# Kernel optimization log

Measured on AMD Instinct MI355X. Metric: run time of the kernel, lower is better.

## Reference

```python
import jax, jax.numpy as jnp
import numpy as np

B, L, D = 4, 1024, 1024
E, H = 8, 4096          # num_experts, mlp hidden = 4*D
CAPACITY = 6            # kthvalue rank factor: expert_k = B*L*CAPACITY


def setup_inputs() -> dict:
    key = jax.random.key(0)
    ks = jax.random.split(key, 6)
    x = jax.random.normal(ks[0], (B, L, D), dtype=jnp.float32)
    gate_weight = jax.random.normal(ks[1], (E, D), dtype=jnp.float32) * 0.006
    w1 = jax.random.normal(ks[2], (E, H, D), dtype=jnp.float32) * 0.02
    b1 = jnp.zeros((E, H), dtype=jnp.float32)
    w2 = jax.random.normal(ks[3], (E, D, H), dtype=jnp.float32) * 0.02
    b2 = jnp.zeros((E, D), dtype=jnp.float32)
    return {"x": x, "gate_weight": gate_weight, "w1": w1, "b1": b1, "w2": w2, "b2": b2}


def reference(x, gate_weight, w1, b1, w2, b2):
    # Router: logits [B, L, E]
    logits = jnp.einsum('bld,ed->ble', x, gate_weight)
    # Global kth-smallest threshold over all B*L*E token-expert logits
    expert_k = B * L * CAPACITY
    kth_val = jnp.sort(logits.reshape(-1))[expert_k - 1]
    mask = (logits >= kth_val).astype(x.dtype)
    gates = logits * mask  # identity gate * boolean mask
    # Dense per-expert MLP on every token: [B, L, E, H] hidden
    h = jax.nn.gelu(jnp.einsum('bld,ehd->bleh', x, w1) + b1, approximate=True)
    # Expert outputs stacked along last dim: [B, L, D, E]
    y = jnp.einsum('bleh,edh->blde', h, w2) + b2.T[None, None]
    # Weighted sum combine over experts
    out = jnp.einsum('blde,ble->bld', y, gates)
    return out
```

## Files before the change

kernel.cpp:

```cpp
#include <hip/hip_runtime.h>
#include <hip/hip_bf16.h>

#define TT 4096
#define DD 1024
#define EE 8
#define HH 4096
#define KSEL 24576
#define HS  1536

using f32x4 = __attribute__((ext_vector_type(4))) float;
using s16x8 = __attribute__((ext_vector_type(8))) short;

__device__ __forceinline__ unsigned short f2bf(float f) {
    unsigned int u = __float_as_uint(f);
    unsigned int r = u + 0x7FFFu + ((u >> 16) & 1u);
    return (unsigned short)(r >> 16);
}

__device__ __forceinline__ float gelu_tanh(float v) {
    float v3 = v * v * v;
    return 0.5f * v * (1.0f + tanhf(0.7978845608028654f * (v + 0.044715f * v3)));
}

__device__ __forceinline__ s16x8 cvt8(float4 a, float4 b) {
    s16x8 r;
    r[0] = (short)f2bf(a.x); r[1] = (short)f2bf(a.y);
    r[2] = (short)f2bf(a.z); r[3] = (short)f2bf(a.w);
    r[4] = (short)f2bf(b.x); r[5] = (short)f2bf(b.y);
    r[6] = (short)f2bf(b.z); r[7] = (short)f2bf(b.w);
    return r;
}

__global__ void k_logits(const float* __restrict__ x, const float* __restrict__ gw,
                         float* __restrict__ logits) {
    int wid = threadIdx.x >> 6, lane = threadIdx.x & 63;
    int t = blockIdx.x * 4 + wid;
    if (t >= TT) return;
    const float* xr = x + (size_t)t * DD;
    float acc[EE];
#pragma unroll
    for (int e = 0; e < EE; ++e) acc[e] = 0.f;
    for (int i = 0; i < DD / 64; ++i) {
        int d = i * 64 + lane;
        float xv = xr[d];
#pragma unroll
        for (int e = 0; e < EE; ++e) acc[e] += xv * gw[e * DD + d];
    }
#pragma unroll
    for (int e = 0; e < EE; ++e) {
        float v = acc[e];
        for (int off = 32; off; off >>= 1) v += __shfl_xor(v, off, 64);
        if (lane == 0) logits[(size_t)t * EE + e] = v;
    }
}

__global__ void k_select(const float* __restrict__ logits, float* __restrict__ kth) {
    int tid = threadIdx.x;
    unsigned int v[32];
#pragma unroll
    for (int i = 0; i < 32; ++i) {
        unsigned int b = __float_as_uint(logits[tid + i * 1024]);
        v[i] = (b & 0x80000000u) ? ~b : (b | 0x80000000u);
    }
    __shared__ int s_cnt;
    unsigned int prefix = 0;
    for (int bit = 31; bit >= 0; --bit) {
        unsigned int cand = prefix | (1u << bit);
        int c = 0;
#pragma unroll
        for (int i = 0; i < 32; ++i) c += (v[i] < cand) ? 1 : 0;
        for (int off = 32; off; off >>= 1) c += __shfl_xor(c, off, 64);
        __syncthreads();
        if (tid == 0) s_cnt = 0;
        __syncthreads();
        if ((tid & 63) == 0) atomicAdd(&s_cnt, c);
        __syncthreads();
        if (s_cnt < KSEL) prefix = cand;
    }
    if (tid == 0) {
        unsigned int b = (prefix & 0x80000000u) ? (prefix ^ 0x80000000u) : ~prefix;
        *kth = __uint_as_float(b);
    }
}

__global__ void k_lists(const float* __restrict__ logits, const float* __restrict__ kth,
                        int* __restrict__ cnt, int* __restrict__ toks,
                        float* __restrict__ gates) {
    int idx = blockIdx.x * 256 + threadIdx.x;
    float v = logits[idx];
    if (v >= *kth) {
        int e = idx & 7, t = idx >> 3;
        int p = atomicAdd(&cnt[e], 1);
        if (p < TT) { toks[e * TT + p] = t; gates[e * TT + p] = v; }
    }
}


#define SWZ_W(r, cb) ((r) * 64 + ((cb) ^ (((r) & 3) << 4)))

__global__ __launch_bounds__(256, 2) void k_mlp1(
    const float* __restrict__ x, const float* __restrict__ w1,
    const float* __restrict__ b1, const int* __restrict__ cnt,
    const int* __restrict__ toks, unsigned short* __restrict__ h_ws) {
    int e = blockIdx.z;
    int c = cnt[e];
    int m0 = blockIdx.x * 128;
    if (m0 >= c) return;
    int n0 = blockIdx.y * 128;

    __shared__ char sA[2][8192];
    __shared__ char sB[2][8192];

    int tid = threadIdx.x;
    int w = tid >> 6, lane = tid & 63;
    int l15 = lane & 15, l4 = lane >> 4;
    int wrow = (w >> 1) * 64, wcol = (w & 1) * 64;

    int ra = tid >> 1, ha = tid & 1;
    int ptok = m0 + ra;
    int tok = (ptok < c) ? toks[e * TT + ptok] : 0;
    const float* srcA = x + (size_t)tok * DD + ha * 16;
    const float* srcB = w1 + ((size_t)e * HH + n0 + ra) * DD + ha * 16;
    int wbyteA0 = SWZ_W(ra, ha * 32);
    int wbyteA1 = SWZ_W(ra, ha * 32 + 16);

    f32x4 acc[4][4];
#pragma unroll
    for (int mf = 0; mf < 4; ++mf)
#pragma unroll
        for (int nf = 0; nf < 4; ++nf) acc[mf][nf] = (f32x4){0.f, 0.f, 0.f, 0.f};

    int rchunk = ((l4 ^ (l15 & 3)) * 16);

    float4 la[4], lb[4];
#pragma unroll
    for (int q = 0; q < 4; ++q) { la[q] = ((const float4*)srcA)[q]; lb[q] = ((const float4*)srcB)[q]; }
    *(s16x8*)(&sA[0][wbyteA0]) = cvt8(la[0], la[1]);
    *(s16x8*)(&sA[0][wbyteA1]) = cvt8(la[2], la[3]);
    *(s16x8*)(&sB[0][wbyteA0]) = cvt8(lb[0], lb[1]);
    *(s16x8*)(&sB[0][wbyteA1]) = cvt8(lb[2], lb[3]);
    __syncthreads();

    const int NS = DD / 32;
    for (int s = 0; s < NS; ++s) {
        if (s + 1 < NS) {
            const float* pa = srcA + (s + 1) * 32;
            const float* pb = srcB + (s + 1) * 32;
#pragma unroll
            for (int q = 0; q < 4; ++q) { la[q] = ((const float4*)pa)[q]; lb[q] = ((const float4*)pb)[q]; }
        }
        int buf = s & 1;
        s16x8 af[4], bf[4];
#pragma unroll
        for (int mf = 0; mf < 4; ++mf) {
            int r = wrow + mf * 16 + l15;
            af[mf] = *(const s16x8*)(&sA[buf][r * 64 + rchunk]);
        }
#pragma unroll
        for (int nf = 0; nf < 4; ++nf) {
            int r = wcol + nf * 16 + l15;
            bf[nf] = *(const s16x8*)(&sB[buf][r * 64 + rchunk]);
        }
#pragma unroll
        for (int mf = 0; mf < 4; ++mf)
#pragma unroll
            for (int nf = 0; nf < 4; ++nf)
                acc[mf][nf] = __builtin_amdgcn_mfma_f32_16x16x32_bf16(af[mf], bf[nf], acc[mf][nf], 0, 0, 0);
        if (s + 1 < NS) {
            int nb = buf ^ 1;
            *(s16x8*)(&sA[nb][wbyteA0]) = cvt8(la[0], la[1]);
            *(s16x8*)(&sA[nb][wbyteA1]) = cvt8(la[2], la[3]);
            *(s16x8*)(&sB[nb][wbyteA0]) = cvt8(lb[0], lb[1]);
            *(s16x8*)(&sB[nb][wbyteA1]) = cvt8(lb[2], lb[3]);
        }
        __syncthreads();
    }

#pragma unroll
    for (int nf = 0; nf < 4; ++nf) {
        int hcol = n0 + wcol + nf * 16 + l15;
        float bias = b1[(size_t)e * HH + hcol];
#pragma unroll
        for (int mf = 0; mf < 4; ++mf) {
#pragma unroll
            for (int j = 0; j < 4; ++j) {
                int p = m0 + wrow + mf * 16 + l4 * 4 + j;
                h_ws[((size_t)e * HS + p) * HH + hcol] = f2bf(gelu_tanh(acc[mf][nf][j] + bias));
            }
        }
    }
}

__global__ __launch_bounds__(256, 2) void k_mlp2(
    const unsigned short* __restrict__ h_ws, const float* __restrict__ w2,
    const float* __restrict__ b2, const int* __restrict__ cnt,
    const int* __restrict__ toks, const float* __restrict__ gates,
    float* __restrict__ out) {
    int e = blockIdx.z;
    int c = cnt[e];
    int m0 = blockIdx.x * 128;
    if (m0 >= c) return;
    int n0 = blockIdx.y * 128;

    __shared__ char sA[2][8192];
    __shared__ char sB[2][8192];
    __shared__ int s_tok[128];
    __shared__ float s_gate[128];

    int tid = threadIdx.x;
    if (tid < 128) {
        int p = m0 + tid;
        s_tok[tid]  = (p < c) ? toks[e * TT + p] : 0;
        s_gate[tid] = (p < c) ? gates[e * TT + p] : 0.f;
    }

    int w = tid >> 6, lane = tid & 63;
    int l15 = lane & 15, l4 = lane >> 4;
    int wrow = (w >> 1) * 64, wcol = (w & 1) * 64;

    int ra = tid >> 1, ha = tid & 1;
    const unsigned short* srcA = h_ws + ((size_t)e * HS + m0 + ra) * HH + ha * 16;
    const float* srcB = w2 + ((size_t)e * DD + n0 + ra) * HH + ha * 16;
    int wbyte0 = SWZ_W(ra, ha * 32);
    int wbyte1 = SWZ_W(ra, ha * 32 + 16);

    f32x4 acc[4][4];
#pragma unroll
    for (int mf = 0; mf < 4; ++mf)
#pragma unroll
        for (int nf = 0; nf < 4; ++nf) acc[mf][nf] = (f32x4){0.f, 0.f, 0.f, 0.f};

    int rchunk = ((l4 ^ (l15 & 3)) * 16);

    s16x8 la0, la1; float4 lb[4];
    la0 = ((const s16x8*)srcA)[0]; la1 = ((const s16x8*)srcA)[1];
#pragma unroll
    for (int q = 0; q < 4; ++q) lb[q] = ((const float4*)srcB)[q];
    *(s16x8*)(&sA[0][wbyte0]) = la0;
    *(s16x8*)(&sA[0][wbyte1]) = la1;
    *(s16x8*)(&sB[0][wbyte0]) = cvt8(lb[0], lb[1]);
    *(s16x8*)(&sB[0][wbyte1]) = cvt8(lb[2], lb[3]);
    __syncthreads();

    const int NS = HH / 32;
    for (int s = 0; s < NS; ++s) {
        if (s + 1 < NS) {
            const unsigned short* pa = srcA + (s + 1) * 32;
            const float* pb = srcB + (s + 1) * 32;
            la0 = ((const s16x8*)pa)[0]; la1 = ((const s16x8*)pa)[1];
#pragma unroll
            for (int q = 0; q < 4; ++q) lb[q] = ((const float4*)pb)[q];
        }
        int buf = s & 1;
        s16x8 af[4], bf[4];
#pragma unroll
        for (int mf = 0; mf < 4; ++mf) {
            int r = wrow + mf * 16 + l15;
            af[mf] = *(const s16x8*)(&sA[buf][r * 64 + rchunk]);
        }
#pragma unroll
        for (int nf = 0; nf < 4; ++nf) {
            int r = wcol + nf * 16 + l15;
            bf[nf] = *(const s16x8*)(&sB[buf][r * 64 + rchunk]);
        }
#pragma unroll
        for (int mf = 0; mf < 4; ++mf)
#pragma unroll
            for (int nf = 0; nf < 4; ++nf)
                acc[mf][nf] = __builtin_amdgcn_mfma_f32_16x16x32_bf16(af[mf], bf[nf], acc[mf][nf], 0, 0, 0);
        if (s + 1 < NS) {
            int nb = buf ^ 1;
            *(s16x8*)(&sA[nb][wbyte0]) = la0;
            *(s16x8*)(&sA[nb][wbyte1]) = la1;
            *(s16x8*)(&sB[nb][wbyte0]) = cvt8(lb[0], lb[1]);
            *(s16x8*)(&sB[nb][wbyte1]) = cvt8(lb[2], lb[3]);
        }
        __syncthreads();
    }

#pragma unroll
    for (int nf = 0; nf < 4; ++nf) {
        int col = n0 + wcol + nf * 16 + l15;
        float bb = b2[(size_t)e * DD + col];
#pragma unroll
        for (int mf = 0; mf < 4; ++mf) {
#pragma unroll
            for (int j = 0; j < 4; ++j) {
                int prow = wrow + mf * 16 + l4 * 4 + j;
                if (m0 + prow < c) {
                    atomicAdd(&out[(size_t)s_tok[prow] * DD + col],
                              s_gate[prow] * (acc[mf][nf][j] + bb));
                }
            }
        }
    }
}

extern "C" void kernel_launch(void* const* d_in, const int* in_sizes, int n_in,
                              void* d_out, int out_size, void* d_ws, size_t ws_size,
                              hipStream_t stream) {
    const float* x  = (const float*)d_in[0];
    const float* gw = (const float*)d_in[1];
    const float* w1 = (const float*)d_in[2];
    const float* b1 = (const float*)d_in[3];
    const float* w2 = (const float*)d_in[4];
    const float* b2 = (const float*)d_in[5];
    float* out = (float*)d_out;

    char* ws = (char*)d_ws;
    float* logits = (float*)ws;
    float* kth    = (float*)(ws + 131072);
    int*   cnt    = (int*)(ws + 131104);
    int*   toks   = (int*)(ws + 131136);
    float* gates  = (float*)(ws + 262208);
    unsigned short* h_ws = (unsigned short*)(ws + 1048576);

    hipMemsetAsync(out, 0, (size_t)TT * DD * sizeof(float), stream);
    hipMemsetAsync(cnt, 0, EE * sizeof(int), stream);

    k_logits<<<dim3(TT / 4), dim3(256), 0, stream>>>(x, gw, logits);
    k_select<<<dim3(1), dim3(1024), 0, stream>>>(logits, kth);
    k_lists<<<dim3(TT * EE / 256), dim3(256), 0, stream>>>(logits, kth, cnt, toks, gates);
    k_mlp1<<<dim3(12, 32, 8), dim3(256), 0, stream>>>(x, w1, b1, cnt, toks, h_ws);
    k_mlp2<<<dim3(12, 8, 8), dim3(256), 0, stream>>>(h_ws, w2, b2, cnt, toks, gates, out);
}
```

Before: 817.0 us.

## Pre-convert weights to bf16 and use direct global-to-LDS loads in expert GEMMs

Adds a conversion pass that writes x, w1 and w2 to bf16 copies in workspace. New GEMM kernels then stream tiles straight into LDS with global_load_lds, which removes per-tile register conversion and staging. The second GEMM is split over two K halves and combined with atomics, and the LDS swizzle pattern is changed. The cost is an extra full pass over the fp32 weights every call, a larger workspace requirement, and a fallback to the old kernels if the workspace is too small.

```diff
diff --git a/kernel.cpp b/kernel.cpp
--- a/kernel.cpp
+++ b/kernel.cpp
@@ -12,9 +12,9 @@
 using s16x8 = __attribute__((ext_vector_type(8))) short;
 
 __device__ __forceinline__ unsigned short f2bf(float f) {
-    unsigned int u = __float_as_uint(f);
-    unsigned int r = u + 0x7FFFu + ((u >> 16) & 1u);
-    return (unsigned short)(r >> 16);
+    union { __hip_bfloat16 h; unsigned short u; } v;
+    v.h = __float2bfloat16(f);
+    return v.u;
 }
 
 __device__ __forceinline__ float gelu_tanh(float v) {
@@ -29,6 +29,12 @@
     r[4] = (short)f2bf(b.x); r[5] = (short)f2bf(b.y);
     r[6] = (short)f2bf(b.z); r[7] = (short)f2bf(b.w);
     return r;
+}
+
+typedef const __attribute__((address_space(1))) unsigned int ga_u32;
+typedef __attribute__((address_space(3))) unsigned int ls_u32;
+__device__ __forceinline__ void gld16(const void* g, void* l) {
+    __builtin_amdgcn_global_load_lds((ga_u32*)g, (ls_u32*)l, 16, 0, 0);
 }
 
 __global__ void k_logits(const float* __restrict__ x, const float* __restrict__ gw,
@@ -95,8 +101,206 @@
     }
 }
 
-
-#define SWZ_W(r, cb) ((r) * 64 + ((cb) ^ (((r) & 3) << 4)))
+__global__ void k_cvt(const float* __restrict__ src, unsigned short* __restrict__ dst, int n8) {
+    int i = blockIdx.x * blockDim.x + threadIdx.x;
+    int stride = gridDim.x * blockDim.x;
+    for (; i < n8; i += stride) {
+        float4 a = ((const float4*)src)[2 * i];
+        float4 b = ((const float4*)src)[2 * i + 1];
+        ((s16x8*)dst)[i] = cvt8(a, b);
+    }
+}
+
+#define SWZ_W(r, cb) ((r) * 64 + ((cb) ^ ((((r) >> 1) & 3) << 4)))
+
+
+__global__ __launch_bounds__(256, 4) void k_mlp1_f(
+    const unsigned short* __restrict__ xb, const unsigned short* __restrict__ w1b,
+    const float* __restrict__ b1, const int* __restrict__ cnt,
+    const int* __restrict__ toks, unsigned short* __restrict__ h_ws) {
+    int e = blockIdx.z;
+    int c = cnt[e];
+    int m0 = blockIdx.x * 128;
+    if (m0 >= c) return;
+    int n0 = blockIdx.y * 128;
+
+    __shared__ unsigned short sA[2][4096];
+    __shared__ unsigned short sB[2][4096];
+    __shared__ int s_tok[128];
+
+    int tid = threadIdx.x;
+    if (tid < 128) {
+        int p = m0 + tid;
+        s_tok[tid] = (p < c) ? toks[e * TT + p] : 0;
+    }
+    __syncthreads();
+
+    int w = tid >> 6, lane = tid & 63;
+    int l15 = lane & 15, l4 = lane >> 4;
+    int wrow = (w >> 1) * 64, wcol = (w & 1) * 64;
+
+    int sr = lane >> 2;
+    int ci = (lane & 3) * 16;
+    int r0 = w * 32 + sr, r1 = r0 + 16;
+    int sw0 = ((r0 >> 1) & 3) << 4, sw1 = ((r1 >> 1) & 3) << 4;
+    const char* gA0 = (const char*)(xb + (size_t)s_tok[r0] * DD) + (ci ^ sw0);
+    const char* gA1 = (const char*)(xb + (size_t)s_tok[r1] * DD) + (ci ^ sw1);
+    const char* gB0 = (const char*)(w1b + ((size_t)e * HH + n0 + r0) * DD) + (ci ^ sw0);
+    const char* gB1 = (const char*)(w1b + ((size_t)e * HH + n0 + r1) * DD) + (ci ^ sw1);
+    char* dA = (char*)&sA[0][0] + w * 2048;
+    char* dB = (char*)&sB[0][0] + w * 2048;
+
+    f32x4 acc[4][4];
+#pragma unroll
+    for (int mf = 0; mf < 4; ++mf)
+#pragma unroll
+        for (int nf = 0; nf < 4; ++nf) acc[mf][nf] = (f32x4){0.f, 0.f, 0.f, 0.f};
+
+    int rchunk = (l4 ^ ((l15 >> 1) & 3)) * 16;
+
+    gld16(gA0, dA); gld16(gA1, dA + 1024);
+    gld16(gB0, dB); gld16(gB1, dB + 1024);
+    __syncthreads();
+
+    const int NS = DD / 32;
+    int buf = 0;
+    for (int s = 0; s < NS; ++s) {
+        if (s + 1 < NS) {
+            int ko = (s + 1) * 64;
+            int nb = buf ^ 1;
+            gld16(gA0 + ko, dA + nb * 8192); gld16(gA1 + ko, dA + nb * 8192 + 1024);
+            gld16(gB0 + ko, dB + nb * 8192); gld16(gB1 + ko, dB + nb * 8192 + 1024);
+        }
+        const char* bA = (const char*)&sA[buf][0];
+        const char* bB = (const char*)&sB[buf][0];
+        s16x8 af[4], bfr[4];
+#pragma unroll
+        for (int mf = 0; mf < 4; ++mf)
+            af[mf] = *(const s16x8*)(bA + (wrow + mf * 16 + l15) * 64 + rchunk);
+#pragma unroll
+        for (int nf = 0; nf < 4; ++nf)
+            bfr[nf] = *(const s16x8*)(bB + (wcol + nf * 16 + l15) * 64 + rchunk);
+#pragma unroll
+        for (int mf = 0; mf < 4; ++mf)
+#pragma unroll
+            for (int nf = 0; nf < 4; ++nf)
+                acc[mf][nf] = __builtin_amdgcn_mfma_f32_16x16x32_bf16(af[mf], bfr[nf], acc[mf][nf], 0, 0, 0);
+        __syncthreads();
+        buf ^= 1;
+    }
+
+#pragma unroll
+    for (int nf = 0; nf < 4; ++nf) {
+        int hcol = n0 + wcol + nf * 16 + l15;
+        float bias = b1[(size_t)e * HH + hcol];
+#pragma unroll
+        for (int mf = 0; mf < 4; ++mf) {
+#pragma unroll
+            for (int j = 0; j < 4; ++j) {
+                int p = m0 + wrow + mf * 16 + l4 * 4 + j;
+                h_ws[((size_t)e * HS + p) * HH + hcol] = f2bf(gelu_tanh(acc[mf][nf][j] + bias));
+            }
+        }
+    }
+}
+
+__global__ __launch_bounds__(256, 4) void k_mlp2_f(
+    const unsigned short* __restrict__ h_ws, const unsigned short* __restrict__ w2b,
+    const float* __restrict__ b2, const int* __restrict__ cnt,
+    const int* __restrict__ toks, const float* __restrict__ gates,
+    float* __restrict__ out) {
+    int e = blockIdx.z;
+    int c = cnt[e];
+    int m0 = blockIdx.x * 128;
+    if (m0 >= c) return;
+    int n0 = (blockIdx.y & 7) * 128;
+    int kz = blockIdx.y >> 3;
+    size_t kbase = (size_t)kz * 2048;
+
+    __shared__ unsigned short sA[2][4096];
+    __shared__ unsigned short sB[2][4096];
+    __shared__ int s_tok[128];
+    __shared__ float s_gate[128];
+
+    int tid = threadIdx.x;
+    if (tid < 128) {
+        int p = m0 + tid;
+        s_tok[tid]  = (p < c) ? toks[e * TT + p] : 0;
+        s_gate[tid] = (p < c) ? gates[e * TT + p] : 0.f;
+    }
+
+    int w = tid >> 6, lane = tid & 63;
+    int l15 = lane & 15, l4 = lane >> 4;
+    int wrow = (w >> 1) * 64, wcol = (w & 1) * 64;
+
+    int sr = lane >> 2;
+    int ci = (lane & 3) * 16;
+    int r0 = w * 32 + sr, r1 = r0 + 16;
+    int sw0 = ((r0 >> 1) & 3) << 4, sw1 = ((r1 >> 1) & 3) << 4;
+    const char* gA0 = (const char*)(h_ws + ((size_t)e * HS + m0 + r0) * HH + kbase) + (ci ^ sw0);
+    const char* gA1 = (const char*)(h_ws + ((size_t)e * HS + m0 + r1) * HH + kbase) + (ci ^ sw1);
+    const char* gB0 = (const char*)(w2b + ((size_t)e * DD + n0 + r0) * HH + kbase) + (ci ^ sw0);
+    const char* gB1 = (const char*)(w2b + ((size_t)e * DD + n0 + r1) * HH + kbase) + (ci ^ sw1);
+    char* dA = (char*)&sA[0][0] + w * 2048;
+    char* dB = (char*)&sB[0][0] + w * 2048;
+
+    f32x4 acc[4][4];
+#pragma unroll
+    for (int mf = 0; mf < 4; ++mf)
+#pragma unroll
+        for (int nf = 0; nf < 4; ++nf) acc[mf][nf] = (f32x4){0.f, 0.f, 0.f, 0.f};
+
+    int rchunk = (l4 ^ ((l15 >> 1) & 3)) * 16;
+
+    gld16(gA0, dA); gld16(gA1, dA + 1024);
+    gld16(gB0, dB); gld16(gB1, dB + 1024);
+    __syncthreads();
+
+    const int NS = 2048 / 32;
+    int buf = 0;
+    for (int s = 0; s < NS; ++s) {
+        if (s + 1 < NS) {
+            int ko = (s + 1) * 64;
+            int nb = buf ^ 1;
+            gld16(gA0 + ko, dA + nb * 8192); gld16(gA1 + ko, dA + nb * 8192 + 1024);
+            gld16(gB0 + ko, dB + nb * 8192); gld16(gB1 + ko, dB + nb * 8192 + 1024);
+        }
+        const char* bA = (const char*)&sA[buf][0];
+        const char* bB = (const char*)&sB[buf][0];
+        s16x8 af[4], bfr[4];
+#pragma unroll
+        for (int mf = 0; mf < 4; ++mf)
+            af[mf] = *(const s16x8*)(bA + (wrow + mf * 16 + l15) * 64 + rchunk);
+#pragma unroll
+        for (int nf = 0; nf < 4; ++nf)
+            bfr[nf] = *(const s16x8*)(bB + (wcol + nf * 16 + l15) * 64 + rchunk);
+#pragma unroll
+        for (int mf = 0; mf < 4; ++mf)
+#pragma unroll
+            for (int nf = 0; nf < 4; ++nf)
+                acc[mf][nf] = __builtin_amdgcn_mfma_f32_16x16x32_bf16(af[mf], bfr[nf], acc[mf][nf], 0, 0, 0);
+        __syncthreads();
+        buf ^= 1;
+    }
+
+#pragma unroll
+    for (int nf = 0; nf < 4; ++nf) {
+        int col = n0 + wcol + nf * 16 + l15;
+        float bb = (kz == 0) ? b2[(size_t)e * DD + col] : 0.f;
+#pragma unroll
+        for (int mf = 0; mf < 4; ++mf) {
+#pragma unroll
+            for (int j = 0; j < 4; ++j) {
+                int prow = wrow + mf * 16 + l4 * 4 + j;
+                if (m0 + prow < c) {
+                    atomicAdd(&out[(size_t)s_tok[prow] * DD + col],
+                              s_gate[prow] * (acc[mf][nf][j] + bb));
+                }
+            }
+        }
+    }
+}
+
 
 __global__ __launch_bounds__(256, 2) void k_mlp1(
     const float* __restrict__ x, const float* __restrict__ w1,
@@ -130,7 +334,7 @@
 #pragma unroll
         for (int nf = 0; nf < 4; ++nf) acc[mf][nf] = (f32x4){0.f, 0.f, 0.f, 0.f};
 
-    int rchunk = ((l4 ^ (l15 & 3)) * 16);
+    int rchunk = (l4 ^ ((l15 >> 1) & 3)) * 16;
 
     float4 la[4], lb[4];
 #pragma unroll
@@ -150,22 +354,18 @@
             for (int q = 0; q < 4; ++q) { la[q] = ((const float4*)pa)[q]; lb[q] = ((const float4*)pb)[q]; }
         }
         int buf = s & 1;
-        s16x8 af[4], bf[4];
-#pragma unroll
-        for (int mf = 0; mf < 4; ++mf) {
-            int r = wrow + mf * 16 + l15;
-            af[mf] = *(const s16x8*)(&sA[buf][r * 64 + rchunk]);
-        }
-#pragma unroll
-        for (int nf = 0; nf < 4; ++nf) {
-            int r = wcol + nf * 16 + l15;
-            bf[nf] = *(const s16x8*)(&sB[buf][r * 64 + rchunk]);
-        }
+        s16x8 af[4], bfr[4];
+#pragma unroll
+        for (int mf = 0; mf < 4; ++mf)
+            af[mf] = *(const s16x8*)(&sA[buf][(wrow + mf * 16 + l15) * 64 + rchunk]);
+#pragma unroll
+        for (int nf = 0; nf < 4; ++nf)
+            bfr[nf] = *(const s16x8*)(&sB[buf][(wcol + nf * 16 + l15) * 64 + rchunk]);
 #pragma unroll
         for (int mf = 0; mf < 4; ++mf)
 #pragma unroll
             for (int nf = 0; nf < 4; ++nf)
-                acc[mf][nf] = __builtin_amdgcn_mfma_f32_16x16x32_bf16(af[mf], bf[nf], acc[mf][nf], 0, 0, 0);
+                acc[mf][nf] = __builtin_amdgcn_mfma_f32_16x16x32_bf16(af[mf], bfr[nf], acc[mf][nf], 0, 0, 0);
         if (s + 1 < NS) {
             int nb = buf ^ 1;
             *(s16x8*)(&sA[nb][wbyteA0]) = cvt8(la[0], la[1]);
@@ -230,7 +430,7 @@
 #pragma unroll
         for (int nf = 0; nf < 4; ++nf) acc[mf][nf] = (f32x4){0.f, 0.f, 0.f, 0.f};
 
-    int rchunk = ((l4 ^ (l15 & 3)) * 16);
+    int rchunk = (l4 ^ ((l15 >> 1) & 3)) * 16;
 
     s16x8 la0, la1; float4 lb[4];
     la0 = ((const s16x8*)srcA)[0]; la1 = ((const s16x8*)srcA)[1];
@@ -252,22 +452,18 @@
             for (int q = 0; q < 4; ++q) lb[q] = ((const float4*)pb)[q];
         }
         int buf = s & 1;
-        s16x8 af[4], bf[4];
-#pragma unroll
-        for (int mf = 0; mf < 4; ++mf) {
-            int r = wrow + mf * 16 + l15;
-            af[mf] = *(const s16x8*)(&sA[buf][r * 64 + rchunk]);
-        }
-#pragma unroll
-        for (int nf = 0; nf < 4; ++nf) {
-            int r = wcol + nf * 16 + l15;
-            bf[nf] = *(const s16x8*)(&sB[buf][r * 64 + rchunk]);
-        }
+        s16x8 af[4], bfr[4];
+#pragma unroll
+        for (int mf = 0; mf < 4; ++mf)
+            af[mf] = *(const s16x8*)(&sA[buf][(wrow + mf * 16 + l15) * 64 + rchunk]);
+#pragma unroll
+        for (int nf = 0; nf < 4; ++nf)
+            bfr[nf] = *(const s16x8*)(&sB[buf][(wcol + nf * 16 + l15) * 64 + rchunk]);
 #pragma unroll
         for (int mf = 0; mf < 4; ++mf)
 #pragma unroll
             for (int nf = 0; nf < 4; ++nf)
-                acc[mf][nf] = __builtin_amdgcn_mfma_f32_16x16x32_bf16(af[mf], bf[nf], acc[mf][nf], 0, 0, 0);
+                acc[mf][nf] = __builtin_amdgcn_mfma_f32_16x16x32_bf16(af[mf], bfr[nf], acc[mf][nf], 0, 0, 0);
         if (s + 1 < NS) {
             int nb = buf ^ 1;
             *(s16x8*)(&sA[nb][wbyte0]) = la0;
@@ -313,7 +509,6 @@
     int*   cnt    = (int*)(ws + 131104);
     int*   toks   = (int*)(ws + 131136);
     float* gates  = (float*)(ws + 262208);
-    unsigned short* h_ws = (unsigned short*)(ws + 1048576);
 
     hipMemsetAsync(out, 0, (size_t)TT * DD * sizeof(float), stream);
     hipMemsetAsync(cnt, 0, EE * sizeof(int), stream);
@@ -321,6 +516,26 @@
     k_logits<<<dim3(TT / 4), dim3(256), 0, stream>>>(x, gw, logits);
     k_select<<<dim3(1), dim3(1024), 0, stream>>>(logits, kth);
     k_lists<<<dim3(TT * EE / 256), dim3(256), 0, stream>>>(logits, kth, cnt, toks, gates);
-    k_mlp1<<<dim3(12, 32, 8), dim3(256), 0, stream>>>(x, w1, b1, cnt, toks, h_ws);
-    k_mlp2<<<dim3(12, 8, 8), dim3(256), 0, stream>>>(h_ws, w2, b2, cnt, toks, gates, out);
-}
+
+    const size_t OFF_XB  = 1048576;
+    const size_t OFF_W1B = OFF_XB + (size_t)TT * DD * 2;
+    const size_t OFF_W2B = OFF_W1B + (size_t)EE * HH * DD * 2;
+    const size_t OFF_H   = OFF_W2B + (size_t)EE * DD * HH * 2;
+    const size_t NEEDED  = OFF_H + (size_t)EE * HS * HH * 2;
+
+    if (ws_size >= NEEDED) {
+        unsigned short* xb   = (unsigned short*)(ws + OFF_XB);
+        unsigned short* w1b  = (unsigned short*)(ws + OFF_W1B);
+        unsigned short* w2b  = (unsigned short*)(ws + OFF_W2B);
+        unsigned short* h_ws = (unsigned short*)(ws + OFF_H);
+        k_cvt<<<dim3(2048), dim3(256), 0, stream>>>(x, xb, TT * DD / 8);
+        k_cvt<<<dim3(2048), dim3(256), 0, stream>>>(w1, w1b, EE * HH * DD / 8);
+        k_cvt<<<dim3(2048), dim3(256), 0, stream>>>(w2, w2b, EE * DD * HH / 8);
+        k_mlp1_f<<<dim3(12, 32, 8), dim3(256), 0, stream>>>(xb, w1b, b1, cnt, toks, h_ws);
+        k_mlp2_f<<<dim3(12, 16, 8), dim3(256), 0, stream>>>(h_ws, w2b, b2, cnt, toks, gates, out);
+    } else {
+        unsigned short* h_ws = (unsigned short*)(ws + 1048576);
+        k_mlp1<<<dim3(12, 32, 8), dim3(256), 0, stream>>>(x, w1, b1, cnt, toks, h_ws);
+        k_mlp2<<<dim3(12, 8, 8), dim3(256), 0, stream>>>(h_ws, w2, b2, cnt, toks, gates, out);
+    }
+}
```

Result: faster. 778.6 us (-4.7%).
